# Performance work log

Hardware: AMD Instinct MI355X
Metric: run time of the kernel (lower is better)

The kernel has to match this reference:

```python
import jax, jax.numpy as jnp
import numpy as np

# Cayley-Dickson octonion multiplication tables (from the source module)
SIGN_TABLE = np.array([
    [+1, -1, -1, -1, -1, -1, -1, -1],
    [+1, +1, +1, -1, +1, -1, -1, +1],
    [+1, -1, +1, +1, +1, +1, -1, -1],
    [+1, +1, -1, +1, +1, -1, +1, -1],
    [+1, -1, -1, -1, +1, +1, +1, +1],
    [+1, +1, -1, +1, -1, +1, -1, +1],
    [+1, +1, +1, -1, -1, +1, +1, -1],
    [+1, -1, +1, +1, -1, -1, +1, +1],
], dtype=np.float32)
WEIGHT_IDX = np.array([
    [0, 1, 2, 3, 4, 5, 6, 7],
    [1, 0, 3, 2, 5, 4, 7, 6],
    [2, 3, 0, 1, 6, 7, 4, 5],
    [3, 2, 1, 0, 7, 6, 5, 4],
    [4, 5, 6, 7, 0, 1, 2, 3],
    [5, 4, 7, 6, 1, 0, 3, 2],
    [6, 7, 4, 5, 2, 3, 0, 1],
    [7, 6, 5, 4, 3, 2, 1, 0],
], dtype=np.int32)

B, T, D_IN, D_OUT = 4, 2048, 4096, 4096
K = D_IN // 8   # per-component input dim
N = D_OUT // 8  # per-component output dim


def setup_inputs() -> dict:
    key = jax.random.key(0)
    k1, k2 = jax.random.split(key)
    x = jax.random.normal(k1, (B, T, D_IN), dtype=jnp.float32)
    weight = jax.random.normal(k2, (8, N, K), dtype=jnp.float32) * (1.0 / np.sqrt(K))
    return {"x": x, "weight": weight}


def reference(x, weight):
    """Fused octonion (Cayley-Dickson) linear layer.

    y_i = sum_j sign[i,j] * x_j @ W[widx[i,j]].T
    x components are contiguous chunks of the last dim: x_j = x[..., j*K:(j+1)*K].
    """
    b, t, f = x.shape
    k = f // 8
    xs = x.reshape(b, t, 8, k)                 # [B,T,8,K], component axis j
    Wg = weight[jnp.asarray(WEIGHT_IDX)]        # [8(i),8(j),N,K] gathered weights
    S = jnp.asarray(SIGN_TABLE, dtype=x.dtype)  # [8(i),8(j)]
    # contract over j (component) and k (features); produce [B,T,i,N]
    y = jnp.einsum('ij,btjk,ijnk->btin', S, xs, Wg)
    return y.reshape(b, t, -1)                  # [B,T,8*N]
```

## Files before the change

### kernel.cpp

```cpp
#include <hip/hip_runtime.h>
#include <stdint.h>

typedef __attribute__((ext_vector_type(8))) short bf16x8;
typedef __attribute__((ext_vector_type(4))) float f32x4;

#define D_IN  4096
#define D_OUT 4096
#define KC 512
#define NC 512
#define NT 64

__constant__ float c_sign[64] = {
 +1,-1,-1,-1,-1,-1,-1,-1,
 +1,+1,+1,-1,+1,-1,-1,+1,
 +1,-1,+1,+1,+1,+1,-1,-1,
 +1,+1,-1,+1,+1,-1,+1,-1,
 +1,-1,-1,-1,+1,+1,+1,+1,
 +1,+1,-1,+1,-1,+1,-1,+1,
 +1,+1,+1,-1,-1,+1,+1,-1,
 +1,-1,+1,+1,-1,-1,+1,+1,
};

__device__ inline unsigned int pack2bf16(float a, float b) {
    unsigned int ua = __builtin_bit_cast(unsigned int, a);
    unsigned int ub = __builtin_bit_cast(unsigned int, b);
    ua = (ua + 0x7FFFu + ((ua >> 16) & 1u)) >> 16;
    ub = (ub + 0x7FFFu + ((ub >> 16) & 1u)) >> 16;
    return ua | (ub << 16);
}

typedef __attribute__((address_space(1))) const unsigned int gas_u32;
typedef __attribute__((address_space(3))) unsigned int las_u32;
#define ASYNC16(g, l) __builtin_amdgcn_global_load_lds((gas_u32*)(g), (las_u32*)(l), 16, 0, 0)


__global__ __launch_bounds__(256)
void conv_x(const float* __restrict__ in, unsigned short* __restrict__ out, int n8) {
    int i = blockIdx.x * blockDim.x + threadIdx.x;
    if (i >= n8) return;
    const float4 a = ((const float4*)in)[(size_t)i * 2];
    const float4 b = ((const float4*)in)[(size_t)i * 2 + 1];
    uint4 o;
    o.x = pack2bf16(a.x, a.y); o.y = pack2bf16(a.z, a.w);
    o.z = pack2bf16(b.x, b.y); o.w = pack2bf16(b.z, b.w);
    ((uint4*)out)[i] = o;
}

__global__ __launch_bounds__(256)
void conv_w(const float* __restrict__ W, unsigned short* __restrict__ out) {
    int gid = blockIdx.x * blockDim.x + threadIdx.x;
    int row = gid >> 9;
    int c8  = gid & 511;
    int i = row >> 9, n = row & 511;
    int j = c8 >> 6;
    int k = (c8 & 63) << 3;
    float sgn = c_sign[i * 8 + j];
    const float* src = W + ((((i ^ j) * NC + n) * KC) + k);
    float4 a = *(const float4*)(src);
    float4 b = *(const float4*)(src + 4);
    uint4 o;
    o.x = pack2bf16(a.x * sgn, a.y * sgn); o.y = pack2bf16(a.z * sgn, a.w * sgn);
    o.z = pack2bf16(b.x * sgn, b.y * sgn); o.w = pack2bf16(b.z * sgn, b.w * sgn);
    ((uint4*)out)[gid] = o;
}


#define ENDP do { __builtin_amdgcn_s_barrier(); asm volatile("" ::: "memory"); } while (0)

__device__ __forceinline__ void read_a(bf16x8 (&d)[4], const unsigned short* buf,
                                       int mh, int kk, int lane, int wr) {
#pragma unroll
    for (int f = 0; f < 4; ++f) {
        const int r  = wr * 128 + (mh * 4 + f) * 16 + (lane & 15);
        const int ch = (kk * 4 + (lane >> 4)) ^ (r & 7);
        d[f] = *(const bf16x8*)((const char*)buf + r * 128 + (ch << 4));
    }
}

__device__ __forceinline__ void read_b(bf16x8 (&d)[4], const unsigned short* buf,
                                       int kk, int lane, int wc) {
#pragma unroll
    for (int n = 0; n < 4; ++n) {
        const int r  = wc * 64 + n * 16 + (lane & 15);
        const int ch = (kk * 4 + (lane >> 4)) ^ (r & 7);
        d[n] = *(const bf16x8*)((const char*)buf + r * 128 + (ch << 4));
    }
}

__device__ __forceinline__ void mfma8(f32x4 (&acc)[8][4], int mh,
                                      const bf16x8 (&a)[4], const bf16x8 (&b)[4]) {
#pragma unroll
    for (int f = 0; f < 4; ++f)
#pragma unroll
        for (int n = 0; n < 4; ++n)
            acc[mh * 4 + f][n] = __builtin_amdgcn_mfma_f32_16x16x32_bf16(
                a[f], b[n], acc[mh * 4 + f][n], 0, 0, 0);
}

__device__ __forceinline__ void ktile(
    const unsigned short* Abuf, const unsigned short* Bbuf,
    f32x4 (&acc)[8][4],
    const unsigned short* sg0, unsigned short* sl0,
    const unsigned short* sg1, unsigned short* sl1,
    const unsigned short* sg2, unsigned short* sl2,
    const unsigned short* sg3, unsigned short* sl3,
    size_t goff0, size_t goff1, int loff0, int loff1,
    int lane, int wr, int wc)
{
    bf16x8 a0[4], a1[4], b0[4], b1[4];
    read_a(a0, Abuf, 0, 0, lane, wr);
    read_b(b0, Bbuf, 0, lane, wc);
    read_b(b1, Bbuf, 1, lane, wc);
    ASYNC16(sg0 + goff0, sl0 + loff0); ASYNC16(sg0 + goff1, sl0 + loff1);
    __builtin_amdgcn_s_barrier();
    __builtin_amdgcn_s_setprio(1);
    mfma8(acc, 0, a0, b0);
    __builtin_amdgcn_s_setprio(0);
    read_a(a1, Abuf, 1, 0, lane, wr);
    ENDP;
    ASYNC16(sg1 + goff0, sl1 + loff0); ASYNC16(sg1 + goff1, sl1 + loff1);
    __builtin_amdgcn_s_barrier();
    __builtin_amdgcn_s_setprio(1);
    mfma8(acc, 1, a1, b0);
    __builtin_amdgcn_s_setprio(0);
    read_a(a0, Abuf, 0, 1, lane, wr);
    ENDP;
    ASYNC16(sg2 + goff0, sl2 + loff0); ASYNC16(sg2 + goff1, sl2 + loff1);
    __builtin_amdgcn_s_barrier();
    __builtin_amdgcn_s_setprio(1);
    mfma8(acc, 0, a0, b1);
    __builtin_amdgcn_s_setprio(0);
    read_a(a1, Abuf, 1, 1, lane, wr);
    ENDP;
    ASYNC16(sg3 + goff0, sl3 + loff0); ASYNC16(sg3 + goff1, sl3 + loff1);
    __builtin_amdgcn_s_barrier();
    __builtin_amdgcn_s_setprio(1);
    mfma8(acc, 1, a1, b1);
    __builtin_amdgcn_s_setprio(0);
}

__global__ __launch_bounds__(512, 2)
void octo_gemm_8ph(const unsigned short* __restrict__ Xb,
                   const unsigned short* __restrict__ Wb,
                   float* __restrict__ Y, int M)
{
    __shared__ __align__(16) unsigned short sm[65536];
    unsigned short* A0 = sm;
    unsigned short* A1 = sm + 16384;
    unsigned short* B0 = sm + 32768;
    unsigned short* B1 = sm + 49152;

    const int tid  = threadIdx.x;
    const int lane = tid & 63;
    const int wave = tid >> 6;
    const int wr   = wave >> 2;
    const int wc   = wave & 3;

    const int nbn = D_OUT / 256;
    const int nwg = (M / 256) * nbn;
    int bid = blockIdx.x;
    int cpx = nwg >> 3;
    int wg  = (bid & 7) * cpx + (bid >> 3);
    const int bm = wg / nbn, bn = wg % nbn;
    const int row0 = bm * 256, col0 = bn * 256;

    const int srow  = tid >> 3;
    const int sch   = tid & 7;
    const size_t goff0 = (size_t)srow * D_IN + (size_t)((sch ^ (srow & 7)) * 8);
    const size_t goff1 = goff0 + (size_t)64 * D_IN;
    const int loff0 = tid * 8;
    const int loff1 = loff0 + 4096;

    const unsigned short* gX = Xb + (size_t)row0 * D_IN;
    const unsigned short* gW = Wb + (size_t)col0 * D_IN;

    f32x4 acc[8][4];
    #pragma unroll
    for (int m = 0; m < 8; ++m)
        #pragma unroll
        for (int n = 0; n < 4; ++n)
            acc[m][n] = (f32x4){0.f, 0.f, 0.f, 0.f};

    ASYNC16(gX + goff0, A0 + loff0);              ASYNC16(gX + goff1, A0 + loff1);
    ASYNC16(gX + 128 * D_IN + goff0, A0 + 8192 + loff0);
    ASYNC16(gX + 128 * D_IN + goff1, A0 + 8192 + loff1);
    ASYNC16(gW + goff0, B0 + loff0);              ASYNC16(gW + goff1, B0 + loff1);
    ASYNC16(gW + 128 * D_IN + goff0, B0 + 8192 + loff0);
    ASYNC16(gW + 128 * D_IN + goff1, B0 + 8192 + loff1);
    ASYNC16(gW + 64 + goff0, B1 + loff0);         ASYNC16(gW + 64 + goff1, B1 + loff1);
    ASYNC16(gW + 64 + 128 * D_IN + goff0, B1 + 8192 + loff0);
    ASYNC16(gW + 64 + 128 * D_IN + goff1, B1 + 8192 + loff1);
    asm volatile("s_waitcnt vmcnt(4)");
    ENDP;

    for (int i = 0; i < NT / 2; ++i) {
        const int u = 2 * i;
        const unsigned short* gA1t = gX + ((u + 1) & (NT - 1)) * 64;
        const unsigned short* gA2t = gX + ((u + 2) & (NT - 1)) * 64;
        const unsigned short* gB2t = gW + ((u + 2) & (NT - 1)) * 64;
        const unsigned short* gB3t = gW + ((u + 3) & (NT - 1)) * 64;

        ktile(A0, B0, acc,
              gA1t,              A1,
              gA1t + 128 * D_IN, A1 + 8192,
              gB2t,              B0,
              gB2t + 128 * D_IN, B0 + 8192,
              goff0, goff1, loff0, loff1, lane, wr, wc);
        asm volatile("s_waitcnt vmcnt(4)");
        ENDP;
        ktile(A1, B1, acc,
              gA2t,              A0,
              gA2t + 128 * D_IN, A0 + 8192,
              gB3t,              B1,
              gB3t + 128 * D_IN, B1 + 8192,
              goff0, goff1, loff0, loff1, lane, wr, wc);
        asm volatile("s_waitcnt vmcnt(4)");
        ENDP;
    }

    const int rl = (lane >> 4) << 2;
    const int cl = lane & 15;
    #pragma unroll
    for (int m = 0; m < 8; ++m) {
        const int rg = row0 + wr * 128 + m * 16 + rl;
        #pragma unroll
        for (int n = 0; n < 4; ++n) {
            const int cg = col0 + wc * 64 + n * 16 + cl;
            #pragma unroll
            for (int q = 0; q < 4; ++q)
                Y[(size_t)(rg + q) * D_OUT + cg] = acc[m][n][q];
        }
    }
}


#define BM 128
#define BN 128
#define BK 64

__global__ __launch_bounds__(256)
void octo_gemm_f32(const float* __restrict__ X, const float* __restrict__ W,
                   float* __restrict__ Y, int M)
{
    __shared__ __align__(16) unsigned short As[BM * BK];
    __shared__ __align__(16) unsigned short Bs[BN * BK];

    const int tid  = threadIdx.x;
    const int lane = tid & 63;
    const int wave = tid >> 6;
    const int wr   = wave >> 1;
    const int wc   = wave & 1;

    const int nbn = D_OUT / BN;
    const int nwg = (M / BM) * nbn;
    int bid = blockIdx.x;
    int wg  = bid;
    if ((nwg & 7) == 0) {
        int cpx = nwg >> 3;
        wg = (bid & 7) * cpx + (bid >> 3);
    }
    const int bm = wg / nbn, bn = wg % nbn;
    const int row0  = bm * BM;
    const int col0  = bn * BN;
    const int icomp = col0 >> 9;
    const int noff  = col0 & (NC - 1);

    const int srow = tid >> 4;
    const int scol = (tid & 15) << 2;

    f32x4 acc[4][4];
    #pragma unroll
    for (int m = 0; m < 4; ++m)
        #pragma unroll
        for (int n = 0; n < 4; ++n)
            acc[m][n] = (f32x4){0.f, 0.f, 0.f, 0.f};

    char* AsB = (char*)As;
    char* BsB = (char*)Bs;
    const int byteC = scol << 1;

    for (int step = 0; step < NT; ++step) {
        const int k0 = step * BK;
        const int j  = k0 >> 9;
        const int kc = k0 & (KC - 1);
        const float sgn = c_sign[icomp * 8 + j];
        const int   w   = icomp ^ j;
        const float* Wp = W + (((size_t)w * NC + noff) * KC + kc);
        const float* Xp = X + ((size_t)row0 * D_IN + k0);

        __syncthreads();
        #pragma unroll
        for (int p = 0; p < 8; ++p) {
            const int r  = p * 16 + srow;
            const int sb = r * 128 + ((((byteC >> 4) ^ (r & 7)) << 4)) + (byteC & 8);
            const float4 va = *(const float4*)(&Xp[(size_t)r * D_IN + scol]);
            *(uint2*)(AsB + sb) = make_uint2(pack2bf16(va.x, va.y),
                                             pack2bf16(va.z, va.w));
            const float4 vb = *(const float4*)(&Wp[(size_t)r * KC + scol]);
            *(uint2*)(BsB + sb) = make_uint2(pack2bf16(vb.x * sgn, vb.y * sgn),
                                             pack2bf16(vb.z * sgn, vb.w * sgn));
        }
        __syncthreads();

        #pragma unroll
        for (int kk = 0; kk < 2; ++kk) {
            bf16x8 af[4], bf[4];
            #pragma unroll
            for (int m = 0; m < 4; ++m) {
                const int r = wr * 64 + m * 16 + (lane & 15);
                const int chunk = (kk * 4 + (lane >> 4)) ^ (r & 7);
                af[m] = *(const bf16x8*)(AsB + r * 128 + (chunk << 4));
            }
            #pragma unroll
            for (int n = 0; n < 4; ++n) {
                const int r = wc * 64 + n * 16 + (lane & 15);
                const int chunk = (kk * 4 + (lane >> 4)) ^ (r & 7);
                bf[n] = *(const bf16x8*)(BsB + r * 128 + (chunk << 4));
            }
            #pragma unroll
            for (int m = 0; m < 4; ++m)
                #pragma unroll
                for (int n = 0; n < 4; ++n)
                    acc[m][n] = __builtin_amdgcn_mfma_f32_16x16x32_bf16(
                        af[m], bf[n], acc[m][n], 0, 0, 0);
        }
    }

    const int rl = (lane >> 4) << 2;
    const int cl = lane & 15;
    #pragma unroll
    for (int m = 0; m < 4; ++m) {
        const int rg = row0 + wr * 64 + m * 16 + rl;
        #pragma unroll
        for (int n = 0; n < 4; ++n) {
            const int cg = col0 + wc * 64 + n * 16 + cl;
            #pragma unroll
            for (int q = 0; q < 4; ++q)
                Y[(size_t)(rg + q) * D_OUT + cg] = acc[m][n][q];
        }
    }
}

extern "C" void kernel_launch(void* const* d_in, const int* in_sizes, int n_in,
                              void* d_out, int out_size, void* d_ws, size_t ws_size,
                              hipStream_t stream) {
    const float* X = (const float*)d_in[0];
    const float* W = (const float*)d_in[1];
    float* Y = (float*)d_out;
    const int M = in_sizes[0] / D_IN;

    const size_t xb_bytes = (size_t)M * D_IN * sizeof(unsigned short);
    const size_t wb_bytes = (size_t)D_OUT * D_IN * sizeof(unsigned short);

    if (ws_size >= xb_bytes + wb_bytes && (M % 256) == 0) {
        unsigned short* Xb = (unsigned short*)d_ws;
        unsigned short* Wb = (unsigned short*)((char*)d_ws + xb_bytes);
        const int n8x = M * D_IN / 8;
        hipLaunchKernelGGL(conv_x, dim3(n8x / 256), dim3(256), 0, stream, X, Xb, n8x);
        hipLaunchKernelGGL(conv_w, dim3((D_OUT * D_IN / 8) / 256), dim3(256), 0, stream, W, Wb);
        const int nwg = (M / 256) * (D_OUT / 256);
        hipLaunchKernelGGL(octo_gemm_8ph, dim3(nwg), dim3(512), 0, stream, Xb, Wb, Y, M);
    } else {
        const int nwg = (M / BM) * (D_OUT / BN);
        hipLaunchKernelGGL(octo_gemm_f32, dim3(nwg), dim3(256), 0, stream, X, W, Y, M);
    }
}
```

Before: 263.3 us.

## Software-pipeline LDS fragment reads across k-tiles with register double buffering

New measurement: 263.3 us. Within noise of the previous version (-0.0%).

```diff
diff --git a/kernel.cpp b/kernel.cpp
--- a/kernel.cpp
+++ b/kernel.cpp
@@ -97,46 +97,51 @@
                 a[f], b[n], acc[mh * 4 + f][n], 0, 0, 0);
 }
 
-__device__ __forceinline__ void ktile(
-    const unsigned short* Abuf, const unsigned short* Bbuf,
+__device__ __forceinline__ void ktile_pipe(
+    const unsigned short* Ac, const unsigned short* Bc,
+    const unsigned short* An, const unsigned short* Bn,
+    unsigned short* stA, unsigned short* stB,
+    const unsigned short* gA1, const unsigned short* gB2,
     f32x4 (&acc)[8][4],
-    const unsigned short* sg0, unsigned short* sl0,
-    const unsigned short* sg1, unsigned short* sl1,
-    const unsigned short* sg2, unsigned short* sl2,
-    const unsigned short* sg3, unsigned short* sl3,
+    bf16x8 (&aX)[4], bf16x8 (&aY)[4], bf16x8 (&bX)[4], bf16x8 (&bY)[4],
     size_t goff0, size_t goff1, int loff0, int loff1,
     int lane, int wr, int wc)
 {
-    bf16x8 a0[4], a1[4], b0[4], b1[4];
-    read_a(a0, Abuf, 0, 0, lane, wr);
-    read_b(b0, Bbuf, 0, lane, wc);
-    read_b(b1, Bbuf, 1, lane, wc);
-    ASYNC16(sg0 + goff0, sl0 + loff0); ASYNC16(sg0 + goff1, sl0 + loff1);
+    read_a(aY, Ac, 1, 0, lane, wr);
+    ASYNC16(gA1 + goff0, stA + loff0);
+    ASYNC16(gA1 + goff1, stA + loff1);
     __builtin_amdgcn_s_barrier();
     __builtin_amdgcn_s_setprio(1);
-    mfma8(acc, 0, a0, b0);
+    mfma8(acc, 0, aX, bX);
     __builtin_amdgcn_s_setprio(0);
-    read_a(a1, Abuf, 1, 0, lane, wr);
-    ENDP;
-    ASYNC16(sg1 + goff0, sl1 + loff0); ASYNC16(sg1 + goff1, sl1 + loff1);
+    ENDP;
+    read_a(aX, Ac, 0, 1, lane, wr);
+    read_b(bY, Bc, 1, lane, wc);
+    ASYNC16(gA1 + 128 * D_IN + goff0, stA + 8192 + loff0);
+    ASYNC16(gA1 + 128 * D_IN + goff1, stA + 8192 + loff1);
     __builtin_amdgcn_s_barrier();
     __builtin_amdgcn_s_setprio(1);
-    mfma8(acc, 1, a1, b0);
+    mfma8(acc, 1, aY, bX);
     __builtin_amdgcn_s_setprio(0);
-    read_a(a0, Abuf, 0, 1, lane, wr);
-    ENDP;
-    ASYNC16(sg2 + goff0, sl2 + loff0); ASYNC16(sg2 + goff1, sl2 + loff1);
+    ENDP;
+    read_a(aY, Ac, 1, 1, lane, wr);
+    ASYNC16(gB2 + goff0, stB + loff0);
+    ASYNC16(gB2 + goff1, stB + loff1);
     __builtin_amdgcn_s_barrier();
     __builtin_amdgcn_s_setprio(1);
-    mfma8(acc, 0, a0, b1);
+    mfma8(acc, 0, aX, bY);
     __builtin_amdgcn_s_setprio(0);
-    read_a(a1, Abuf, 1, 1, lane, wr);
-    ENDP;
-    ASYNC16(sg3 + goff0, sl3 + loff0); ASYNC16(sg3 + goff1, sl3 + loff1);
+    asm volatile("s_waitcnt vmcnt(2)");
+    ENDP;
+    read_a(aX, An, 0, 0, lane, wr);
+    read_b(bX, Bn, 0, lane, wc);
+    ASYNC16(gB2 + 128 * D_IN + goff0, stB + 8192 + loff0);
+    ASYNC16(gB2 + 128 * D_IN + goff1, stB + 8192 + loff1);
     __builtin_amdgcn_s_barrier();
     __builtin_amdgcn_s_setprio(1);
-    mfma8(acc, 1, a1, b1);
+    mfma8(acc, 1, aY, bY);
     __builtin_amdgcn_s_setprio(0);
+    ENDP;
 }
 
 __global__ __launch_bounds__(512, 2)
@@ -193,6 +198,10 @@
     asm volatile("s_waitcnt vmcnt(4)");
     ENDP;
 
+    bf16x8 aX[4], aY[4], bX[4], bY[4];
+    read_a(aX, A0, 0, 0, lane, wr);
+    read_b(bX, B0, 0, lane, wc);
+
     for (int i = 0; i < NT / 2; ++i) {
         const int u = 2 * i;
         const unsigned short* gA1t = gX + ((u + 1) & (NT - 1)) * 64;
@@ -200,22 +209,12 @@
         const unsigned short* gB2t = gW + ((u + 2) & (NT - 1)) * 64;
         const unsigned short* gB3t = gW + ((u + 3) & (NT - 1)) * 64;
 
-        ktile(A0, B0, acc,
-              gA1t,              A1,
-              gA1t + 128 * D_IN, A1 + 8192,
-              gB2t,              B0,
-              gB2t + 128 * D_IN, B0 + 8192,
-              goff0, goff1, loff0, loff1, lane, wr, wc);
-        asm volatile("s_waitcnt vmcnt(4)");
-        ENDP;
-        ktile(A1, B1, acc,
-              gA2t,              A0,
-              gA2t + 128 * D_IN, A0 + 8192,
-              gB3t,              B1,
-              gB3t + 128 * D_IN, B1 + 8192,
-              goff0, goff1, loff0, loff1, lane, wr, wc);
-        asm volatile("s_waitcnt vmcnt(4)");
-        ENDP;
+        ktile_pipe(A0, B0, A1, B1, A1, B0, gA1t, gB2t,
+                   acc, aX, aY, bX, bY,
+                   goff0, goff1, loff0, loff1, lane, wr, wc);
+        ktile_pipe(A1, B1, A0, B0, A0, B1, gA2t, gB3t,
+                   acc, aX, aY, bX, bY,
+                   goff0, goff1, loff0, loff1, lane, wr, wc);
     }
 
     const int rl = (lane >> 4) << 2;
```
